# Kernel optimization log

Hardware: AMD Instinct MI355X
Metric: run time of the kernel (lower is better)

The kernel has to match this reference:

```python
import jax, jax.numpy as jnp
import numpy as np

B, C, H, W_DIM = 32, 512, 56, 56
C_INTER = C // 2
EPS = 1e-5


def _conv1x1(x, w, b):
    # 1x1 conv == per-pixel matmul over channels. w: [out, in], b: [out]
    return jnp.einsum('bchw,oc->bohw', x, w) + b[None, :, None, None]


def setup_inputs() -> dict:
    key = jax.random.key(0)
    ks = jax.random.split(key, 5)
    s_in = 1.0 / np.sqrt(C)
    s_mid = 1.0 / np.sqrt(C_INTER)
    return {
        'x': jax.random.normal(ks[0], (B, C, H, W_DIM), dtype=jnp.float32),
        'g_w': jax.random.normal(ks[1], (C_INTER, C), dtype=jnp.float32) * s_in,
        'g_b': jnp.zeros((C_INTER,), dtype=jnp.float32),
        'theta_w': jax.random.normal(ks[2], (C_INTER, C), dtype=jnp.float32) * s_in,
        'theta_b': jnp.zeros((C_INTER,), dtype=jnp.float32),
        'phi_w': jax.random.normal(ks[3], (C_INTER, C), dtype=jnp.float32) * s_in,
        'phi_b': jnp.zeros((C_INTER,), dtype=jnp.float32),
        'W_w': jax.random.normal(ks[4], (C, C_INTER), dtype=jnp.float32) * s_mid,
        'W_b': jnp.zeros((C,), dtype=jnp.float32),
        'gamma': jnp.ones((C,), dtype=jnp.float32),
        'beta': jnp.zeros((C,), dtype=jnp.float32),
    }


def reference(x, g_w, g_b, theta_w, theta_b, phi_w, phi_b, W_w, W_b, gamma, beta):
    b, c, h, w = x.shape
    n = h * w
    g_x = _conv1x1(x, g_w, g_b).reshape(b, C_INTER, n)        # [B, C', N]
    theta_x = _conv1x1(x, theta_w, theta_b).reshape(b, C_INTER, n)
    phi_x = _conv1x1(x, phi_w, phi_b).reshape(b, C_INTER, n)
    # f = theta @ phi^T / N : small [B, C', C'] channel Gram matrix
    f_div_C = jnp.einsum('bcn,bdn->bcd', theta_x, phi_x) / n
    y = jnp.einsum('bcd,bdn->bcn', f_div_C, g_x).reshape(b, C_INTER, h, w)
    z = _conv1x1(y, W_w, W_b) + x
    # BatchNorm2d (training mode): normalize with batch stats over (B,H,W)
    mean = jnp.mean(z, axis=(0, 2, 3), keepdims=True)
    var = jnp.var(z, axis=(0, 2, 3), keepdims=True)
    z_hat = (z - mean) * jax.lax.rsqrt(var + EPS)
    return z_hat * gamma[None, :, None, None] + beta[None, :, None, None]
```

## Files before the change

kernel.cpp:

```cpp
#include <hip/hip_runtime.h>

#define Bn   32
#define Cc   512
#define CIc  256
#define Nsp  3136
#define Npad 3200
#define EPSbn 1e-5f

typedef __attribute__((ext_vector_type(8))) short v8s;
typedef __attribute__((ext_vector_type(4))) float v4f;

__device__ __forceinline__ unsigned short f2bf(float f) {
    unsigned int u = __builtin_bit_cast(unsigned int, f);
    u += 0x7fffu + ((u >> 16) & 1u);
    return (unsigned short)(u >> 16);
}

__device__ __forceinline__ void async16(const unsigned short* g, unsigned short* l) {
    __builtin_amdgcn_global_load_lds(
        (const __attribute__((address_space(1))) unsigned int*)g,
        (__attribute__((address_space(3))) unsigned int*)l, 16, 0, 0);
}

template <int EPI>
__global__ __launch_bounds__(256)
void mfma_gemm(const unsigned short* __restrict__ A, int lda, long a_bs,
               const unsigned short* __restrict__ B, int ldb, long b_bs,
               void* __restrict__ Out, int ldo, long o_bs,
               int K, float scale,
               const float* __restrict__ biasN, const float* __restrict__ biasM,
               const float* __restrict__ xres,
               float* __restrict__ stats, const float* __restrict__ mstd,
               const float* __restrict__ gamma, const float* __restrict__ beta)
{
    __shared__ __align__(16) unsigned short As[128 * 32];
    __shared__ __align__(16) unsigned short Bs[128 * 32];

    const int tid  = threadIdx.x;
    const int w    = tid >> 6;
    const int lane = tid & 63;
    const int b    = blockIdx.z;
    const int m0   = blockIdx.x * 128;
    const int n0   = blockIdx.y * 128;

    const unsigned short* Ab = A + (long)b * a_bs;
    const unsigned short* Bb = B + (long)b * b_bs;

    const int ldrow = 32 * w + (lane >> 2);
    const int ldk   = (lane & 3) * 8;
    unsigned short* lA0 = &As[(2 * w + 0) * 512];
    unsigned short* lA1 = &As[(2 * w + 1) * 512];
    unsigned short* lB0 = &Bs[(2 * w + 0) * 512];
    unsigned short* lB1 = &Bs[(2 * w + 1) * 512];
    const size_t aoff0 = (size_t)(m0 + ldrow) * lda + ldk;
    const size_t aoff1 = aoff0 + (size_t)16 * lda;
    const size_t boff0 = (size_t)(n0 + ldrow) * ldb + ldk;
    const size_t boff1 = boff0 + (size_t)16 * ldb;

    const int wm = (w & 1) * 64;
    const int wn = (w >> 1) * 64;
    const int fr = lane & 15;
    const int fk = (lane >> 4) * 8;

    v4f acc[4][4] = {};

    for (int k0 = 0; k0 < K; k0 += 32) {
        __syncthreads();
        async16(Ab + aoff0 + k0, lA0);
        async16(Ab + aoff1 + k0, lA1);
        async16(Bb + boff0 + k0, lB0);
        async16(Bb + boff1 + k0, lB1);
        __syncthreads();

        v8s af[4], bf[4];
#pragma unroll
        for (int i = 0; i < 4; ++i)
            af[i] = *(const v8s*)&As[(wm + i * 16 + fr) * 32 + fk];
#pragma unroll
        for (int j = 0; j < 4; ++j)
            bf[j] = *(const v8s*)&Bs[(wn + j * 16 + fr) * 32 + fk];
#pragma unroll
        for (int i = 0; i < 4; ++i)
#pragma unroll
            for (int j = 0; j < 4; ++j)
                acc[i][j] = __builtin_amdgcn_mfma_f32_16x16x32_bf16(af[i], bf[j], acc[i][j], 0, 0, 0);
    }

    const int em = wm + ((lane >> 4) << 2);
    const int en = wn + fr;

    if constexpr (EPI == 0) {
        unsigned short* O = (unsigned short*)Out;
#pragma unroll
        for (int j = 0; j < 4; ++j) {
            const int gn = n0 + en + j * 16;
            const float bN = biasN ? biasN[gn] : 0.0f;
            unsigned short* orow = O + (long)b * o_bs + (size_t)gn * ldo + m0 + em;
#pragma unroll
            for (int i = 0; i < 4; ++i) {
                float4 bm = make_float4(0.f, 0.f, 0.f, 0.f);
                if (biasM) bm = *(const float4*)&biasM[m0 + em + i * 16];
                ushort4 o4;
                o4.x = f2bf(acc[i][j].x * scale + bN + bm.x);
                o4.y = f2bf(acc[i][j].y * scale + bN + bm.y);
                o4.z = f2bf(acc[i][j].z * scale + bN + bm.z);
                o4.w = f2bf(acc[i][j].w * scale + bN + bm.w);
                *(ushort4*)&orow[i * 16] = o4;
            }
        }
    } else if constexpr (EPI == 2) {
        float sj[4] = {0.f, 0.f, 0.f, 0.f}, qj[4] = {0.f, 0.f, 0.f, 0.f};
#pragma unroll
        for (int j = 0; j < 4; ++j) {
            const int gc = n0 + en + j * 16;
            const float wb = biasN[gc];
            const float* xrow = xres + (size_t)b * Cc * Nsp + (size_t)gc * Nsp;
#pragma unroll
            for (int i = 0; i < 4; ++i) {
                const int gsp = m0 + em + i * 16;
                if (gsp < Nsp) {
                    const float4 xr = *(const float4*)&xrow[gsp];
                    const float z0 = acc[i][j].x + wb + xr.x;
                    const float z1 = acc[i][j].y + wb + xr.y;
                    const float z2 = acc[i][j].z + wb + xr.z;
                    const float z3 = acc[i][j].w + wb + xr.w;
                    sj[j] += z0 + z1 + z2 + z3;
                    qj[j] += z0 * z0 + z1 * z1 + z2 * z2 + z3 * z3;
                }
            }
        }
        __syncthreads();
        float* red = (float*)As;
        const int cid = (lane >> 4) + ((w & 1) << 2);
#pragma unroll
        for (int j = 0; j < 4; ++j) {
            const int cc = wn + fr + j * 16;
            red[cc * 8 + cid] = sj[j];
            red[1024 + cc * 8 + cid] = qj[j];
        }
        __syncthreads();
        if (tid < 128) {
            float s = 0.f, q = 0.f;
#pragma unroll
            for (int t = 0; t < 8; ++t) { s += red[tid * 8 + t]; q += red[1024 + tid * 8 + t]; }
            atomicAdd(&stats[n0 + tid], s);
            atomicAdd(&stats[Cc + n0 + tid], q);
        }
    } else {
        float* O = (float*)Out;
#pragma unroll
        for (int j = 0; j < 4; ++j) {
            const int gc = n0 + en + j * 16;
            const float a1 = mstd[Cc + gc] * gamma[gc];
            const float a0 = beta[gc] - mstd[gc] * a1 + biasN[gc] * a1;
            const float* xrow = xres + (size_t)b * Cc * Nsp + (size_t)gc * Nsp;
            float* orow = O + (long)b * o_bs + (size_t)gc * (size_t)ldo;
#pragma unroll
            for (int i = 0; i < 4; ++i) {
                const int gsp = m0 + em + i * 16;
                if (gsp < Nsp) {
                    const float4 xr = *(const float4*)&xrow[gsp];
                    float4 o;
                    o.x = (acc[i][j].x + xr.x) * a1 + a0;
                    o.y = (acc[i][j].y + xr.y) * a1 + a0;
                    o.z = (acc[i][j].z + xr.z) * a1 + a0;
                    o.w = (acc[i][j].w + xr.w) * a1 + a0;
                    *(float4*)&orow[gsp] = o;
                }
            }
        }
    }
}

__global__ __launch_bounds__(256)
void cast_transpose(const float* __restrict__ x, unsigned short* __restrict__ xT)
{
    __shared__ float tile[64][65];
    const int b  = blockIdx.z;
    const int n0 = blockIdx.x * 64;
    const int c0 = blockIdx.y * 64;
    const float* xb = x + (size_t)b * Cc * Nsp;
    const int t = threadIdx.x;
    const int tr  = t >> 4;
    const int tc4 = (t & 15) * 4;
#pragma unroll
    for (int i = 0; i < 4; ++i) {
        const int c = tr + i * 16;
        const float4 v = *(const float4*)&xb[(size_t)(c0 + c) * Nsp + n0 + tc4];
        tile[tc4 + 0][c] = v.x;
        tile[tc4 + 1][c] = v.y;
        tile[tc4 + 2][c] = v.z;
        tile[tc4 + 3][c] = v.w;
    }
    __syncthreads();
    unsigned short* xo = xT + (size_t)b * Nsp * Cc;
#pragma unroll
    for (int i = 0; i < 4; ++i) {
        const int n = tr + i * 16;
        ushort4 o;
        o.x = f2bf(tile[n][tc4 + 0]);
        o.y = f2bf(tile[n][tc4 + 1]);
        o.z = f2bf(tile[n][tc4 + 2]);
        o.w = f2bf(tile[n][tc4 + 3]);
        *(ushort4*)&xo[(size_t)(n0 + n) * Cc + c0 + tc4] = o;
    }
}

__global__ void cast_w(const float* __restrict__ src, unsigned short* __restrict__ dst, int n)
{
    const int i = (blockIdx.x * 256 + threadIdx.x) * 4;
    if (i < n) {
        const float4 v = *(const float4*)&src[i];
        ushort4 o;
        o.x = f2bf(v.x); o.y = f2bf(v.y); o.z = f2bf(v.z); o.w = f2bf(v.w);
        *(ushort4*)&dst[i] = o;
    }
}

__global__ void finalize_stats(const float* __restrict__ stats, float* __restrict__ mstd)
{
    const int c = threadIdx.x;
    const float inv = 1.0f / (float)((long)Bn * Nsp);
    const float mean = stats[c] * inv;
    const float var  = stats[Cc + c] * inv - mean * mean;
    mstd[c] = mean;
    mstd[Cc + c] = rsqrtf(var + EPSbn);
}

extern "C" void kernel_launch(void* const* d_in, const int* in_sizes, int n_in,
                              void* d_out, int out_size, void* d_ws, size_t ws_size,
                              hipStream_t stream)
{
    const float* x     = (const float*)d_in[0];
    const float* g_w   = (const float*)d_in[1];
    const float* g_b   = (const float*)d_in[2];
    const float* th_w  = (const float*)d_in[3];
    const float* th_b  = (const float*)d_in[4];
    const float* ph_w  = (const float*)d_in[5];
    const float* ph_b  = (const float*)d_in[6];
    const float* W_w   = (const float*)d_in[7];
    const float* W_b   = (const float*)d_in[8];
    const float* gamma = (const float*)d_in[9];
    const float* beta  = (const float*)d_in[10];
    float* out = (float*)d_out;

    unsigned short* xT = (unsigned short*)d_ws;
    unsigned short* T  = xT + (size_t)Bn * Nsp * Cc;
    unsigned short* P  = T + (size_t)Bn * CIc * Npad;
    unsigned short* F  = P + (size_t)Bn * CIc * Npad;
    unsigned short* w16 = F + (size_t)Bn * CIc * CIc;
    unsigned short* thw16 = w16;
    unsigned short* phw16 = w16 + 131072;
    unsigned short* gw16  = w16 + 2 * 131072;
    unsigned short* Ww16  = w16 + 3 * 131072;
    float* stats = (float*)(w16 + 4 * 131072);
    float* mstd  = stats + 2 * Cc;

    unsigned short* G = T;
    unsigned short* Y = P;

    hipMemsetAsync(stats, 0, 2 * Cc * sizeof(float), stream);

    const dim3 blk(256);
    const long xT_bs = (long)Nsp * Cc;
    const long nc_bs = (long)CIc * Npad;
    const long nh_bs = (long)Npad * CIc;

    cast_transpose<<<dim3(49, 8, Bn), blk, 0, stream>>>(x, xT);
    cast_w<<<dim3(128), blk, 0, stream>>>(th_w, thw16, 131072);
    cast_w<<<dim3(128), blk, 0, stream>>>(ph_w, phw16, 131072);
    cast_w<<<dim3(128), blk, 0, stream>>>(g_w,  gw16,  131072);
    cast_w<<<dim3(128), blk, 0, stream>>>(W_w,  Ww16,  131072);

    mfma_gemm<0><<<dim3(25, 2, Bn), blk, 0, stream>>>(
        xT, Cc, xT_bs, thw16, Cc, 0, T, Npad, nc_bs, Cc, 1.0f,
        th_b, nullptr, nullptr, nullptr, nullptr, nullptr, nullptr);
    mfma_gemm<0><<<dim3(25, 2, Bn), blk, 0, stream>>>(
        xT, Cc, xT_bs, phw16, Cc, 0, P, Npad, nc_bs, Cc, 1.0f,
        ph_b, nullptr, nullptr, nullptr, nullptr, nullptr, nullptr);
    mfma_gemm<0><<<dim3(2, 2, Bn), blk, 0, stream>>>(
        P, Npad, nc_bs, T, Npad, nc_bs, F, CIc, (long)CIc * CIc, Nsp, 1.0f / (float)Nsp,
        nullptr, nullptr, nullptr, nullptr, nullptr, nullptr, nullptr);
    mfma_gemm<0><<<dim3(2, 25, Bn), blk, 0, stream>>>(
        gw16, Cc, 0, xT, Cc, xT_bs, G, CIc, nh_bs, Cc, 1.0f,
        nullptr, g_b, nullptr, nullptr, nullptr, nullptr, nullptr);
    mfma_gemm<0><<<dim3(2, 25, Bn), blk, 0, stream>>>(
        F, CIc, (long)CIc * CIc, G, CIc, nh_bs, Y, CIc, nh_bs, CIc, 1.0f,
        nullptr, nullptr, nullptr, nullptr, nullptr, nullptr, nullptr);
    mfma_gemm<2><<<dim3(25, 4, Bn), blk, 0, stream>>>(
        Y, CIc, nh_bs, Ww16, CIc, 0, nullptr, 0, 0, CIc, 1.0f,
        W_b, nullptr, x, stats, nullptr, nullptr, nullptr);
    finalize_stats<<<dim3(1), dim3(Cc), 0, stream>>>(stats, mstd);
    mfma_gemm<3><<<dim3(25, 4, Bn), blk, 0, stream>>>(
        Y, CIc, nh_bs, Ww16, CIc, 0, out, Nsp, (long)Cc * Nsp, CIc, 1.0f,
        W_b, nullptr, x, nullptr, mstd, gamma, beta);
}
```

Measured before the change: 882.8 us.

## Fold F into g weights, merge theta/phi GEMMs, store z for BN apply

Merges the theta and phi projections into one GEMM with concatenated weights and bias. Folds the Gram matrix F into the g projection by forming a per-batch F·Wg product with a folded bias, so the separate G GEMM and its intermediate buffer go away. The stats GEMM now writes z as bf16, and a lightweight elementwise kernel applies BatchNorm, instead of recomputing the whole W GEMM. This trades extra bf16 rounding of z and per-batch weight products for fewer large GEMMs and less intermediate traffic.

```diff
diff --git a/kernel.cpp b/kernel.cpp
--- a/kernel.cpp
+++ b/kernel.cpp
@@ -16,6 +16,11 @@
     return (unsigned short)(u >> 16);
 }
 
+__device__ __forceinline__ float bf2f(unsigned short u) {
+    unsigned int x = ((unsigned int)u) << 16;
+    return __builtin_bit_cast(float, x);
+}
+
 __device__ __forceinline__ void async16(const unsigned short* g, unsigned short* l) {
     __builtin_amdgcn_global_load_lds(
         (const __attribute__((address_space(1))) unsigned int*)g,
@@ -28,10 +33,9 @@
                const unsigned short* __restrict__ B, int ldb, long b_bs,
                void* __restrict__ Out, int ldo, long o_bs,
                int K, float scale,
-               const float* __restrict__ biasN, const float* __restrict__ biasM,
+               const float* __restrict__ biasN, long bN_bs,
                const float* __restrict__ xres,
-               float* __restrict__ stats, const float* __restrict__ mstd,
-               const float* __restrict__ gamma, const float* __restrict__ beta)
+               float* __restrict__ stats)
 {
     __shared__ __align__(16) unsigned short As[128 * 32];
     __shared__ __align__(16) unsigned short Bs[128 * 32];
@@ -94,27 +98,27 @@
 #pragma unroll
         for (int j = 0; j < 4; ++j) {
             const int gn = n0 + en + j * 16;
-            const float bN = biasN ? biasN[gn] : 0.0f;
+            const float bN = biasN ? biasN[bN_bs * b + gn] : 0.0f;
             unsigned short* orow = O + (long)b * o_bs + (size_t)gn * ldo + m0 + em;
 #pragma unroll
             for (int i = 0; i < 4; ++i) {
-                float4 bm = make_float4(0.f, 0.f, 0.f, 0.f);
-                if (biasM) bm = *(const float4*)&biasM[m0 + em + i * 16];
                 ushort4 o4;
-                o4.x = f2bf(acc[i][j].x * scale + bN + bm.x);
-                o4.y = f2bf(acc[i][j].y * scale + bN + bm.y);
-                o4.z = f2bf(acc[i][j].z * scale + bN + bm.z);
-                o4.w = f2bf(acc[i][j].w * scale + bN + bm.w);
+                o4.x = f2bf(acc[i][j].x * scale + bN);
+                o4.y = f2bf(acc[i][j].y * scale + bN);
+                o4.z = f2bf(acc[i][j].z * scale + bN);
+                o4.w = f2bf(acc[i][j].w * scale + bN);
                 *(ushort4*)&orow[i * 16] = o4;
             }
         }
-    } else if constexpr (EPI == 2) {
+    } else {
+        unsigned short* O = (unsigned short*)Out;
         float sj[4] = {0.f, 0.f, 0.f, 0.f}, qj[4] = {0.f, 0.f, 0.f, 0.f};
 #pragma unroll
         for (int j = 0; j < 4; ++j) {
             const int gc = n0 + en + j * 16;
             const float wb = biasN[gc];
             const float* xrow = xres + (size_t)b * Cc * Nsp + (size_t)gc * Nsp;
+            unsigned short* zrow = O + (long)b * o_bs + (size_t)gc * ldo;
 #pragma unroll
             for (int i = 0; i < 4; ++i) {
                 const int gsp = m0 + em + i * 16;
@@ -126,6 +130,9 @@
                     const float z3 = acc[i][j].w + wb + xr.w;
                     sj[j] += z0 + z1 + z2 + z3;
                     qj[j] += z0 * z0 + z1 * z1 + z2 * z2 + z3 * z3;
+                    ushort4 o4;
+                    o4.x = f2bf(z0); o4.y = f2bf(z1); o4.z = f2bf(z2); o4.w = f2bf(z3);
+                    *(ushort4*)&zrow[gsp] = o4;
                 }
             }
         }
@@ -146,29 +153,6 @@
             atomicAdd(&stats[n0 + tid], s);
             atomicAdd(&stats[Cc + n0 + tid], q);
         }
-    } else {
-        float* O = (float*)Out;
-#pragma unroll
-        for (int j = 0; j < 4; ++j) {
-            const int gc = n0 + en + j * 16;
-            const float a1 = mstd[Cc + gc] * gamma[gc];
-            const float a0 = beta[gc] - mstd[gc] * a1 + biasN[gc] * a1;
-            const float* xrow = xres + (size_t)b * Cc * Nsp + (size_t)gc * Nsp;
-            float* orow = O + (long)b * o_bs + (size_t)gc * (size_t)ldo;
-#pragma unroll
-            for (int i = 0; i < 4; ++i) {
-                const int gsp = m0 + em + i * 16;
-                if (gsp < Nsp) {
-                    const float4 xr = *(const float4*)&xrow[gsp];
-                    float4 o;
-                    o.x = (acc[i][j].x + xr.x) * a1 + a0;
-                    o.y = (acc[i][j].y + xr.y) * a1 + a0;
-                    o.z = (acc[i][j].z + xr.z) * a1 + a0;
-                    o.w = (acc[i][j].w + xr.w) * a1 + a0;
-                    *(float4*)&orow[gsp] = o;
-                }
-            }
-        }
     }
 }
 
@@ -217,6 +201,23 @@
     }
 }
 
+__global__ void cast_wT(const float* __restrict__ src, unsigned short* __restrict__ dst)
+{
+    const int c = blockIdx.x;
+    const int d = threadIdx.x;
+    dst[(size_t)c * CIc + d] = f2bf(src[(size_t)d * Cc + c]);
+}
+
+__global__ void fgb_kernel(const unsigned short* __restrict__ F, const float* __restrict__ g_b,
+                           float* __restrict__ Fgb)
+{
+    const int b = blockIdx.x, cp = threadIdx.x;
+    const unsigned short* Fr = F + ((size_t)b * CIc + cp) * CIc;
+    float acc = 0.f;
+    for (int d = 0; d < CIc; ++d) acc += bf2f(Fr[d]) * g_b[d];
+    Fgb[(size_t)b * CIc + cp] = acc;
+}
+
 __global__ void finalize_stats(const float* __restrict__ stats, float* __restrict__ mstd)
 {
     const int c = threadIdx.x;
@@ -225,6 +226,32 @@
     const float var  = stats[Cc + c] * inv - mean * mean;
     mstd[c] = mean;
     mstd[Cc + c] = rsqrtf(var + EPSbn);
+}
+
+__global__ __launch_bounds__(256)
+void bnorm_apply(const unsigned short* __restrict__ z, const float* __restrict__ mstd,
+                 const float* __restrict__ gamma, const float* __restrict__ beta,
+                 float* __restrict__ out)
+{
+    const int NG = Bn * Cc * (Nsp / 8);
+    const int g = blockIdx.x * 256 + threadIdx.x;
+    if (g >= NG) return;
+    const int c = (g / (Nsp / 8)) & (Cc - 1);
+    const float a1 = mstd[Cc + c] * gamma[c];
+    const float a0 = beta[c] - mstd[c] * a1;
+    const v8s zv = *(const v8s*)(z + (size_t)g * 8);
+    float* op = out + (size_t)g * 8;
+    float4 o0, o1;
+    o0.x = bf2f((unsigned short)zv[0]) * a1 + a0;
+    o0.y = bf2f((unsigned short)zv[1]) * a1 + a0;
+    o0.z = bf2f((unsigned short)zv[2]) * a1 + a0;
+    o0.w = bf2f((unsigned short)zv[3]) * a1 + a0;
+    o1.x = bf2f((unsigned short)zv[4]) * a1 + a0;
+    o1.y = bf2f((unsigned short)zv[5]) * a1 + a0;
+    o1.z = bf2f((unsigned short)zv[6]) * a1 + a0;
+    o1.w = bf2f((unsigned short)zv[7]) * a1 + a0;
+    *(float4*)op = o0;
+    *(float4*)(op + 4) = o1;
 }
 
 extern "C" void kernel_launch(void* const* d_in, const int* in_sizes, int n_in,
@@ -244,54 +271,54 @@
     const float* beta  = (const float*)d_in[10];
     float* out = (float*)d_out;
 
-    unsigned short* xT = (unsigned short*)d_ws;
-    unsigned short* T  = xT + (size_t)Bn * Nsp * Cc;
-    unsigned short* P  = T + (size_t)Bn * CIc * Npad;
-    unsigned short* F  = P + (size_t)Bn * CIc * Npad;
-    unsigned short* w16 = F + (size_t)Bn * CIc * CIc;
-    unsigned short* thw16 = w16;
-    unsigned short* phw16 = w16 + 131072;
-    unsigned short* gw16  = w16 + 2 * 131072;
-    unsigned short* Ww16  = w16 + 3 * 131072;
-    float* stats = (float*)(w16 + 4 * 131072);
-    float* mstd  = stats + 2 * Cc;
-
-    unsigned short* G = T;
-    unsigned short* Y = P;
+    unsigned short* xT  = (unsigned short*)d_ws;
+    unsigned short* T2  = xT + (size_t)Bn * Nsp * Cc;
+    unsigned short* F   = T2 + (size_t)Bn * Cc * Npad;
+    unsigned short* FG  = F + (size_t)Bn * CIc * CIc;
+    unsigned short* thph16 = FG + (size_t)Bn * CIc * Cc;
+    unsigned short* gwT16  = thph16 + Cc * Cc;
+    unsigned short* Ww16   = gwT16 + Cc * CIc;
+    float* thph_b = (float*)(Ww16 + Cc * CIc);
+    float* Fgb    = thph_b + Cc;
+    float* stats  = Fgb + Bn * CIc;
+    float* mstd   = stats + 2 * Cc;
+
+    unsigned short* Y   = T2;
+    unsigned short* z16 = xT;
 
     hipMemsetAsync(stats, 0, 2 * Cc * sizeof(float), stream);
+    hipMemcpyAsync(thph_b, th_b, CIc * sizeof(float), hipMemcpyDeviceToDevice, stream);
+    hipMemcpyAsync(thph_b + CIc, ph_b, CIc * sizeof(float), hipMemcpyDeviceToDevice, stream);
 
     const dim3 blk(256);
     const long xT_bs = (long)Nsp * Cc;
-    const long nc_bs = (long)CIc * Npad;
-    const long nh_bs = (long)Npad * CIc;
+    const long t2_bs = (long)Cc * Npad;
+    const long y_bs  = (long)Npad * CIc;
 
     cast_transpose<<<dim3(49, 8, Bn), blk, 0, stream>>>(x, xT);
-    cast_w<<<dim3(128), blk, 0, stream>>>(th_w, thw16, 131072);
-    cast_w<<<dim3(128), blk, 0, stream>>>(ph_w, phw16, 131072);
-    cast_w<<<dim3(128), blk, 0, stream>>>(g_w,  gw16,  131072);
-    cast_w<<<dim3(128), blk, 0, stream>>>(W_w,  Ww16,  131072);
-
-    mfma_gemm<0><<<dim3(25, 2, Bn), blk, 0, stream>>>(
-        xT, Cc, xT_bs, thw16, Cc, 0, T, Npad, nc_bs, Cc, 1.0f,
-        th_b, nullptr, nullptr, nullptr, nullptr, nullptr, nullptr);
-    mfma_gemm<0><<<dim3(25, 2, Bn), blk, 0, stream>>>(
-        xT, Cc, xT_bs, phw16, Cc, 0, P, Npad, nc_bs, Cc, 1.0f,
-        ph_b, nullptr, nullptr, nullptr, nullptr, nullptr, nullptr);
+    cast_w<<<dim3(128), blk, 0, stream>>>(th_w, thph16, 131072);
+    cast_w<<<dim3(128), blk, 0, stream>>>(ph_w, thph16 + 131072, 131072);
+    cast_w<<<dim3(128), blk, 0, stream>>>(W_w, Ww16, 131072);
+    cast_wT<<<dim3(Cc), dim3(CIc), 0, stream>>>(g_w, gwT16);
+
+    mfma_gemm<0><<<dim3(25, 4, Bn), blk, 0, stream>>>(
+        xT, Cc, xT_bs, thph16, Cc, 0, T2, Npad, t2_bs, Cc, 1.0f,
+        thph_b, 0, nullptr, nullptr);
     mfma_gemm<0><<<dim3(2, 2, Bn), blk, 0, stream>>>(
-        P, Npad, nc_bs, T, Npad, nc_bs, F, CIc, (long)CIc * CIc, Nsp, 1.0f / (float)Nsp,
-        nullptr, nullptr, nullptr, nullptr, nullptr, nullptr, nullptr);
+        T2 + (size_t)CIc * Npad, Npad, t2_bs, T2, Npad, t2_bs,
+        F, CIc, (long)CIc * CIc, Nsp, 1.0f / (float)Nsp,
+        nullptr, 0, nullptr, nullptr);
+    mfma_gemm<0><<<dim3(4, 2, Bn), blk, 0, stream>>>(
+        gwT16, CIc, 0, F, CIc, (long)CIc * CIc, FG, Cc, (long)CIc * Cc, CIc, 1.0f,
+        nullptr, 0, nullptr, nullptr);
+    fgb_kernel<<<dim3(Bn), dim3(CIc), 0, stream>>>(F, g_b, Fgb);
     mfma_gemm<0><<<dim3(2, 25, Bn), blk, 0, stream>>>(
-        gw16, Cc, 0, xT, Cc, xT_bs, G, CIc, nh_bs, Cc, 1.0f,
-        nullptr, g_b, nullptr, nullptr, nullptr, nullptr, nullptr);
-    mfma_gemm<0><<<dim3(2, 25, Bn), blk, 0, stream>>>(
-        F, CIc, (long)CIc * CIc, G, CIc, nh_bs, Y, CIc, nh_bs, CIc, 1.0f,
-        nullptr, nullptr, nullptr, nullptr, nullptr, nullptr, nullptr);
+        FG, Cc, (long)CIc * Cc, xT, Cc, xT_bs, Y, CIc, y_bs, Cc, 1.0f,
+        Fgb, CIc, nullptr, nullptr);
     mfma_gemm<2><<<dim3(25, 4, Bn), blk, 0, stream>>>(
-        Y, CIc, nh_bs, Ww16, CIc, 0, nullptr, 0, 0, CIc, 1.0f,
-        W_b, nullptr, x, stats, nullptr, nullptr, nullptr);
+        Y, CIc, y_bs, Ww16, CIc, 0, z16, Nsp, (long)Cc * Nsp, CIc, 1.0f,
+        W_b, 0, x, stats);
     finalize_stats<<<dim3(1), dim3(Cc), 0, stream>>>(stats, mstd);
-    mfma_gemm<3><<<dim3(25, 4, Bn), blk, 0, stream>>>(
-        Y, CIc, nh_bs, Ww16, CIc, 0, out, Nsp, (long)Cc * Nsp, CIc, 1.0f,
-        W_b, nullptr, x, nullptr, mstd, gamma, beta);
-}
+    bnorm_apply<<<dim3((Bn * Cc * (Nsp / 8) + 255) / 256), blk, 0, stream>>>(
+        z16, mstd, gamma, beta, out);
+}
```

After: 794.9 us. -10.0%, faster.
